# Performance work log

Hardware: AMD Instinct MI355X
Metric: run time of the kernel (lower is better)

The kernel has to match this reference:

```python
import jax, jax.numpy as jnp
import numpy as np

B, C_IN, C_OUT, H, W, K = 8, 32, 32, 96, 96, 5


def setup_inputs() -> dict:
    key = jax.random.key(0)
    k1, k2 = jax.random.split(key)
    f = jax.random.normal(k1, (B, C_IN, H, W), dtype=jnp.float32)
    # xavier_uniform-style init for the structuring element h
    fan_in = C_IN * K * K
    fan_out = C_OUT * K * K
    bound = float(np.sqrt(6.0 / (fan_in + fan_out)))
    h = jax.random.uniform(k2, (C_OUT, C_IN, K, K), dtype=jnp.float32,
                           minval=-bound, maxval=bound)
    return {"f": f, "h": h}


def reference(f, h):
    """Morphological max-plus dilation with 'same' padding.

    out[b,o,y,x] = max_{c,i,j} f[b,c,y+i-p, x+j-p] + h[o,c,i,j]
    """
    b, c, hh, ww = f.shape
    o, _, k, _ = h.shape
    p = k // 2
    neg = -jnp.finfo(f.dtype).max / 2
    fp = jnp.pad(f, ((0, 0), (0, 0), (p, p), (p, p)), constant_values=neg)
    out = jnp.full((b, o, hh, ww), neg, dtype=f.dtype)
    for i in range(k):          # fixed small kernel loop (k*k = 25 taps)
        for j in range(k):
            sl = fp[:, :, i:i + hh, j:j + ww]              # (B, C, H, W)
            w_ij = h[:, :, i, j]                            # (O, C)
            # max-plus over input channels: (B,1,C,H,W) + (O,C,1,1)
            cand = jnp.max(sl[:, None] + w_ij[None, :, :, None, None], axis=2)
            out = jnp.maximum(out, cand)
    return out
```

## Files before the change

kernel.cpp:

```cpp
#include <hip/hip_runtime.h>


#define B_ 8
#define C_ 32
#define O_ 32
#define H_ 96
#define W_ 96
#define K_ 5
#define KK_ (K_ * K_)
#define NCP_ (C_ / 2)

#define TX_ 24
#define RT_ 8
#define CS_ 2
#define TY_ (RT_ * CS_)
#define NT_ (TX_ * TY_)
#define XR_ 4
#define OB_ 4
#define CPG_ (NCP_ / CS_)

#define PH_ 100
#define PW_ 104
#define PLSZ_ (PH_ * PW_)
#define FPAD_BYTES ((size_t)B_ * NCP_ * PLSZ_ * 4)

#define HBLK_ 128
#define HPH_ 24
#define HPACK_DW (8 * NCP_ * HBLK_)

#define NEGF (-30000.0f)

typedef _Float16 h2 __attribute__((ext_vector_type(2)));
typedef int sv8 __attribute__((ext_vector_type(8)));
typedef int sv4 __attribute__((ext_vector_type(4)));
typedef unsigned uv4 __attribute__((ext_vector_type(4)));

static __device__ __forceinline__ h2 h2b(unsigned u) {
    return __builtin_bit_cast(h2, u);
}
static __device__ __forceinline__ unsigned bh2(h2 v) {
    return __builtin_bit_cast(unsigned, v);
}

static __device__ __forceinline__ void pk_addmax_s(h2& acc, h2 fv, int hs) {
    h2 t;
    asm("v_pk_add_f16 %0, %1, %2" : "=v"(t) : "v"(fv), "s"(hs));
    asm("v_pk_max_f16 %0, %1, %2" : "=v"(acc) : "v"(acc), "v"(t));
}

static __device__ __forceinline__ int hget20(sv8 a, sv8 b, sv4 c, int n) {
    if (n < 8)  return a[n];
    if (n < 16) return b[n - 8];
    return c[n - 16];
}

static __device__ __forceinline__ h2 getwin(uv4 a, uv4 b, int d) {
    if (d == 0) return h2b(a[0]);
    if (d == 1) return h2b(a[1]);
    if (d == 2) return h2b(a[2]);
    if (d == 3) return h2b(a[3]);
    if (d == 4) return h2b(b[0]);
    if (d == 5) return h2b(b[1]);
    if (d == 6) return h2b(b[2]);
    return h2b(b[3]);
}

static __device__ __forceinline__ void compute_phase(h2 (&acc)[OB_][XR_],
        uv4 wa, uv4 wb, sv8 c0, sv8 c1, sv4 c2) {
#pragma unroll
    for (int j = 0; j < K_; ++j) {
        const int n = j * 4;
        const int h0 = hget20(c0, c1, c2, n);
        const int h1 = hget20(c0, c1, c2, n + 1);
        const int h2v = hget20(c0, c1, c2, n + 2);
        const int h3 = hget20(c0, c1, c2, n + 3);
#pragma unroll
        for (int xx = 0; xx < XR_; ++xx) {
            h2 fv = getwin(wa, wb, xx + j);
            pk_addmax_s(acc[0][xx], fv, h0);
            pk_addmax_s(acc[1][xx], fv, h1);
            pk_addmax_s(acc[2][xx], fv, h2v);
            pk_addmax_s(acc[3][xx], fv, h3);
        }
    }
}

#define HLOADM(B0, B1, B2, HP, O0S, O1S, O2S)                          \
    asm volatile("s_load_dwordx8 %0, %3, " O0S "\n\t"                  \
                 "s_load_dwordx8 %1, %3, " O1S "\n\t"                  \
                 "s_load_dwordx4 %2, %3, " O2S                         \
                 : "=s"(B0), "=s"(B1), "=s"(B2) : "s"(HP))

#define WLOADM(SA, SB, PTR)                                            \
    asm volatile("global_load_dwordx4 %0, %2, off\n\t"                 \
                 "global_load_dwordx4 %1, %2, off offset:16"           \
                 : "=v"(SA), "=v"(SB) : "v"(PTR))

#define PHASE(CB0, CB1, CB2, NB0, NB1, NB2, NHP, O0S, O1S, O2S, WS, PS, PPTR) \
    do {                                                                      \
        asm volatile("s_waitcnt lgkmcnt(0)"                                   \
                     : "+s"(CB0), "+s"(CB1), "+s"(CB2));                      \
        HLOADM(NB0, NB1, NB2, NHP, O0S, O1S, O2S);                            \
        asm volatile("s_waitcnt vmcnt(6)"                                     \
                     : "+v"(win[WS][0]), "+v"(win[WS][1]));                   \
        WLOADM(win[PS][0], win[PS][1], PPTR);                                 \
        compute_phase(acc, win[WS][0], win[WS][1], CB0, CB1, CB2);            \
    } while (0)

__global__ __launch_bounds__(256)
void prep_kernel(const float* __restrict__ f, const float* __restrict__ h,
                 unsigned* __restrict__ fpad, unsigned* __restrict__ hpack) {
    const int bz = blockIdx.z;
    if (bz < B_) {
        const int idx = blockIdx.x * 256 + threadIdx.x;
        const int cp = blockIdx.y;
        if (idx >= PLSZ_) return;
        const int row = idx / PW_;
        const int col = idx - row * PW_;
        const int y = row - 2;
        const int x = col - 2;
        float v0 = NEGF, v1 = NEGF;
        if ((unsigned)y < H_ && (unsigned)x < W_) {
            v0 = f[((size_t)(bz * C_ + 2 * cp)     * H_ + y) * W_ + x];
            v1 = f[((size_t)(bz * C_ + 2 * cp + 1) * H_ + y) * W_ + x];
        }
        h2 d; d.x = (_Float16)v0; d.y = (_Float16)v1;
        fpad[(size_t)(bz * NCP_ + cp) * PLSZ_ + idx] = bh2(d);
    } else {
        const int t = (blockIdx.y * gridDim.x + blockIdx.x) * 256 + threadIdx.x;
        if (t >= 8 * NCP_ * KK_ * OB_) return;
        const int og = t / (NCP_ * KK_ * OB_);
        int r  = t - og * (NCP_ * KK_ * OB_);
        const int cp = r / (KK_ * OB_);
        r -= cp * (KK_ * OB_);
        const int ij = r / OB_;
        const int o  = r - ij * OB_;
        const int p  = ij / K_;
        const int jj = ij - p * K_;
        float a0 = h[((size_t)(og * OB_ + o) * C_ + 2 * cp)     * KK_ + ij];
        float a1 = h[((size_t)(og * OB_ + o) * C_ + 2 * cp + 1) * KK_ + ij];
        h2 pv; pv.x = (_Float16)a0; pv.y = (_Float16)a1;
        hpack[(size_t)(og * NCP_ + cp) * HBLK_ + p * HPH_ + jj * 4 + o] = bh2(pv);
    }
}

__global__ __launch_bounds__(NT_)
void dilate_main(const unsigned* __restrict__ fpad,
                 const unsigned* __restrict__ hpack,
                 float* __restrict__ out) {
    const int tx  = threadIdx.x;
    const int ty  = threadIdx.y;
    const int ry  = ty & (RT_ - 1);
    const int g   = ty >> 3;
    const int gu  = __builtin_amdgcn_readfirstlane(g);

    const int ytile = blockIdx.x;
    const int og    = blockIdx.y;
    const int b     = blockIdx.z;
    const int y0 = ytile * RT_;
    const int o0 = og * OB_;
    const int x0 = XR_ * tx;
    const int yb = y0 + ry;

    __shared__ unsigned short comb[OB_ * XR_][RT_ * TX_];

    h2 acc[OB_][XR_];
    {
        h2 neg; neg.x = (_Float16)NEGF; neg.y = (_Float16)NEGF;
#pragma unroll
        for (int o = 0; o < OB_; ++o)
#pragma unroll
            for (int xx = 0; xx < XR_; ++xx) acc[o][xx] = neg;
    }

    const int cp0v = g * CPG_;
    const int cp0s = gu * CPG_;
    const unsigned* hpb = hpack + (size_t)(og * NCP_ + cp0s) * HBLK_;
    const unsigned* pvb = fpad + (size_t)(b * NCP_ + cp0v) * PLSZ_ + yb * PW_ + x0;

    sv8 hA0, hA1; sv4 hA2;
    sv8 hB0, hB1; sv4 hB2;
    uv4 win[5][2];

    HLOADM(hA0, hA1, hA2, hpb, "0x0", "0x20", "0x40");
    WLOADM(win[0][0], win[0][1], pvb);
    WLOADM(win[1][0], win[1][1], pvb + PW_);
    WLOADM(win[2][0], win[2][1], pvb + 2 * PW_);
    WLOADM(win[3][0], win[3][1], pvb + 3 * PW_);

#pragma unroll 1
    for (int cpi = 0; cpi < CPG_; cpi += 2) {
        const unsigned* hb0 = hpb + (size_t)cpi * HBLK_;
        const unsigned* hb1 = hb0 + HBLK_;
        const unsigned* hb2 = (cpi + 2 < CPG_) ? hb1 + HBLK_ : hb1;
        const unsigned* pv0 = pvb + (size_t)cpi * PLSZ_;
        const unsigned* pv1 = pv0 + PLSZ_;
        const unsigned* pv2 = (cpi + 2 < CPG_) ? pv1 + PLSZ_ : pv1;

        PHASE(hA0,hA1,hA2, hB0,hB1,hB2, hb0, "0x60","0x80","0xa0",   0, 4, pv0 + 4*PW_);
        PHASE(hB0,hB1,hB2, hA0,hA1,hA2, hb0, "0xc0","0xe0","0x100",  1, 0, pv1);
        PHASE(hA0,hA1,hA2, hB0,hB1,hB2, hb0, "0x120","0x140","0x160",2, 1, pv1 + PW_);
        PHASE(hB0,hB1,hB2, hA0,hA1,hA2, hb0, "0x180","0x1a0","0x1c0",3, 2, pv1 + 2*PW_);
        PHASE(hA0,hA1,hA2, hB0,hB1,hB2, hb1, "0x0","0x20","0x40",    4, 3, pv1 + 3*PW_);
        PHASE(hB0,hB1,hB2, hA0,hA1,hA2, hb1, "0x60","0x80","0xa0",   0, 4, pv1 + 4*PW_);
        PHASE(hA0,hA1,hA2, hB0,hB1,hB2, hb1, "0xc0","0xe0","0x100",  1, 0, pv2);
        PHASE(hB0,hB1,hB2, hA0,hA1,hA2, hb1, "0x120","0x140","0x160",2, 1, pv2 + PW_);
        PHASE(hA0,hA1,hA2, hB0,hB1,hB2, hb1, "0x180","0x1a0","0x1c0",3, 2, pv2 + 2*PW_);
        PHASE(hB0,hB1,hB2, hA0,hA1,hA2, hb2, "0x0","0x20","0x40",    4, 3, pv2 + 3*PW_);
    }

    asm volatile("s_waitcnt vmcnt(0) lgkmcnt(0)"
                 : "+v"(win[0][0]), "+v"(win[0][1]),
                   "+v"(win[1][0]), "+v"(win[1][1]),
                   "+v"(win[2][0]), "+v"(win[2][1]),
                   "+v"(win[3][0]), "+v"(win[3][1]),
                   "+s"(hA0), "+s"(hA1), "+s"(hA2));

    unsigned short red[OB_][XR_];
#pragma unroll
    for (int o = 0; o < OB_; ++o)
#pragma unroll
        for (int xx = 0; xx < XR_; ++xx) {
            _Float16 a = acc[o][xx].x;
            _Float16 b2 = acc[o][xx].y;
            _Float16 m = (a > b2) ? a : b2;
            red[o][xx] = __builtin_bit_cast(unsigned short, m);
        }

    const int t192 = ry * TX_ + tx;
    if (g == 1) {
#pragma unroll
        for (int o = 0; o < OB_; ++o)
#pragma unroll
            for (int xx = 0; xx < XR_; ++xx)
                comb[o * XR_ + xx][t192] = red[o][xx];
    }
    __syncthreads();
    if (g == 0) {
        const int y = yb;
#pragma unroll
        for (int o = 0; o < OB_; ++o) {
            float r[XR_];
#pragma unroll
            for (int xx = 0; xx < XR_; ++xx) {
                _Float16 m  = __builtin_bit_cast(_Float16, red[o][xx]);
                _Float16 v0 = __builtin_bit_cast(_Float16,
                                                 comb[o * XR_ + xx][t192]);
                m = (v0 > m) ? v0 : m;
                r[xx] = (float)m;
            }
            float4 v = make_float4(r[0], r[1], r[2], r[3]);
            *(float4*)&out[(((size_t)b * O_ + (o0 + o)) * H_ + y) * W_ + x0] = v;
        }
    }
}

__global__ __launch_bounds__(256)
void dilate_naive(const float* __restrict__ f, const float* __restrict__ h,
                  float* __restrict__ out) {
    const int idx = blockIdx.x * 256 + threadIdx.x;
    if (idx >= B_ * O_ * H_ * W_) return;
    const int x = idx % W_;
    const int y = (idx / W_) % H_;
    const int o = (idx / (W_ * H_)) % O_;
    const int b = idx / (W_ * H_ * O_);
    float m = -3.0e38f;
    for (int c = 0; c < C_; ++c)
        for (int i = 0; i < K_; ++i)
            for (int j = 0; j < K_; ++j) {
                int yy = y + i - 2, xc = x + j - 2;
                if ((unsigned)yy < H_ && (unsigned)xc < W_) {
                    float v = f[((size_t)(b * C_ + c) * H_ + yy) * W_ + xc] +
                              h[((size_t)o * C_ + c) * KK_ + i * K_ + j];
                    m = fmaxf(m, v);
                }
            }
    out[idx] = m;
}

extern "C" void kernel_launch(void* const* d_in, const int* in_sizes, int n_in,
                              void* d_out, int out_size, void* d_ws, size_t ws_size,
                              hipStream_t stream) {
    const float* f = (const float*)d_in[0];
    const float* h = (const float*)d_in[1];
    float* out = (float*)d_out;

    const size_t need = FPAD_BYTES + (size_t)HPACK_DW * 4;
    if (ws_size >= need) {
        unsigned* fpad  = (unsigned*)d_ws;
        unsigned* hpack = (unsigned*)((char*)d_ws + FPAD_BYTES);
        dim3 pgrid((PLSZ_ + 255) / 256, NCP_, B_ + 1);
        hipLaunchKernelGGL(prep_kernel, pgrid, dim3(256), 0, stream,
                           f, h, fpad, hpack);
        dim3 mgrid(H_ / RT_, O_ / OB_, B_);
        dim3 mblock(TX_, TY_);
        hipLaunchKernelGGL(dilate_main, mgrid, mblock, 0, stream,
                           fpad, hpack, out);
    } else {
        hipLaunchKernelGGL(dilate_naive,
                           dim3((B_ * O_ * H_ * W_ + 255) / 256), dim3(256),
                           0, stream, f, h, out);
    }
}
```

Baseline: 139.5 us.

## Halve output-channel block, shrink window buffering to double-buffer, raise occupancy

Cuts outputs per thread from 4 to 2 channels, doubling the grid along output groups, and replaces the five-deep row-window ring with a two-buffer ping-pong that issues only one row ahead. Loads now use immediate offsets, and the add and max steps are split so adds can be batched. A launch-bounds occupancy hint of 7 is added. The goal is fewer registers and more waves per CU to hide latency, at the cost of loading each input window twice as often across blocks and a shallower prefetch distance.

```diff
diff --git a/kernel.cpp b/kernel.cpp
--- a/kernel.cpp
+++ b/kernel.cpp
@@ -16,7 +16,8 @@
 #define TY_ (RT_ * CS_)
 #define NT_ (TX_ * TY_)
 #define XR_ 4
-#define OB_ 4
+#define OB_ 2
+#define NOG_ (O_ / OB_)
 #define CPG_ (NCP_ / CS_)
 
 #define PH_ 100
@@ -25,14 +26,14 @@
 #define FPAD_BYTES ((size_t)B_ * NCP_ * PLSZ_ * 4)
 
 #define HBLK_ 128
-#define HPH_ 24
-#define HPACK_DW (8 * NCP_ * HBLK_)
+#define HPH_ 16
+#define HPACK_DW (NOG_ * NCP_ * HBLK_)
 
 #define NEGF (-30000.0f)
 
 typedef _Float16 h2 __attribute__((ext_vector_type(2)));
 typedef int sv8 __attribute__((ext_vector_type(8)));
-typedef int sv4 __attribute__((ext_vector_type(4)));
+typedef int sv2 __attribute__((ext_vector_type(2)));
 typedef unsigned uv4 __attribute__((ext_vector_type(4)));
 
 static __device__ __forceinline__ h2 h2b(unsigned u) {
@@ -42,16 +43,18 @@
     return __builtin_bit_cast(unsigned, v);
 }
 
-static __device__ __forceinline__ void pk_addmax_s(h2& acc, h2 fv, int hs) {
+static __device__ __forceinline__ h2 pk_add_s(h2 fv, int hs) {
     h2 t;
     asm("v_pk_add_f16 %0, %1, %2" : "=v"(t) : "v"(fv), "s"(hs));
+    return t;
+}
+static __device__ __forceinline__ void pk_max(h2& acc, h2 t) {
     asm("v_pk_max_f16 %0, %1, %2" : "=v"(acc) : "v"(acc), "v"(t));
 }
 
-static __device__ __forceinline__ int hget20(sv8 a, sv8 b, sv4 c, int n) {
-    if (n < 8)  return a[n];
-    if (n < 16) return b[n - 8];
-    return c[n - 16];
+static __device__ __forceinline__ int hget10(sv8 a, sv2 b, int n) {
+    if (n < 8) return a[n];
+    return b[n - 8];
 }
 
 static __device__ __forceinline__ h2 getwin(uv4 a, uv4 b, int d) {
@@ -66,45 +69,43 @@
 }
 
 static __device__ __forceinline__ void compute_phase(h2 (&acc)[OB_][XR_],
-        uv4 wa, uv4 wb, sv8 c0, sv8 c1, sv4 c2) {
+        uv4 wa, uv4 wb, sv8 c0, sv2 c1) {
 #pragma unroll
     for (int j = 0; j < K_; ++j) {
-        const int n = j * 4;
-        const int h0 = hget20(c0, c1, c2, n);
-        const int h1 = hget20(c0, c1, c2, n + 1);
-        const int h2v = hget20(c0, c1, c2, n + 2);
-        const int h3 = hget20(c0, c1, c2, n + 3);
+        const int h0 = hget10(c0, c1, j * 2);
+        const int h1 = hget10(c0, c1, j * 2 + 1);
+        h2 t[XR_][OB_];
 #pragma unroll
         for (int xx = 0; xx < XR_; ++xx) {
             h2 fv = getwin(wa, wb, xx + j);
-            pk_addmax_s(acc[0][xx], fv, h0);
-            pk_addmax_s(acc[1][xx], fv, h1);
-            pk_addmax_s(acc[2][xx], fv, h2v);
-            pk_addmax_s(acc[3][xx], fv, h3);
-        }
-    }
-}
-
-#define HLOADM(B0, B1, B2, HP, O0S, O1S, O2S)                          \
-    asm volatile("s_load_dwordx8 %0, %3, " O0S "\n\t"                  \
-                 "s_load_dwordx8 %1, %3, " O1S "\n\t"                  \
-                 "s_load_dwordx4 %2, %3, " O2S                         \
-                 : "=s"(B0), "=s"(B1), "=s"(B2) : "s"(HP))
-
-#define WLOADM(SA, SB, PTR)                                            \
-    asm volatile("global_load_dwordx4 %0, %2, off\n\t"                 \
-                 "global_load_dwordx4 %1, %2, off offset:16"           \
+            t[xx][0] = pk_add_s(fv, h0);
+            t[xx][1] = pk_add_s(fv, h1);
+        }
+#pragma unroll
+        for (int xx = 0; xx < XR_; ++xx) {
+            pk_max(acc[0][xx], t[xx][0]);
+            pk_max(acc[1][xx], t[xx][1]);
+        }
+    }
+}
+
+#define HLOADM(B0, B1, HP, O0S, O1S)                                   \
+    asm volatile("s_load_dwordx8 %0, %2, " O0S "\n\t"                  \
+                 "s_load_dwordx2 %1, %2, " O1S                         \
+                 : "=s"(B0), "=s"(B1) : "s"(HP))
+
+#define WLOADM(SA, SB, PTR, O0S, O1S)                                  \
+    asm volatile("global_load_dwordx4 %0, %2, off offset:" O0S "\n\t"  \
+                 "global_load_dwordx4 %1, %2, off offset:" O1S         \
                  : "=v"(SA), "=v"(SB) : "v"(PTR))
 
-#define PHASE(CB0, CB1, CB2, NB0, NB1, NB2, NHP, O0S, O1S, O2S, WS, PS, PPTR) \
-    do {                                                                      \
-        asm volatile("s_waitcnt lgkmcnt(0)"                                   \
-                     : "+s"(CB0), "+s"(CB1), "+s"(CB2));                      \
-        HLOADM(NB0, NB1, NB2, NHP, O0S, O1S, O2S);                            \
-        asm volatile("s_waitcnt vmcnt(6)"                                     \
-                     : "+v"(win[WS][0]), "+v"(win[WS][1]));                   \
-        WLOADM(win[PS][0], win[PS][1], PPTR);                                 \
-        compute_phase(acc, win[WS][0], win[WS][1], CB0, CB1, CB2);            \
+#define PHASE(CH0, CH1, NH0, NH1, NHP, HO0, HO1, CW, NW, NPTR, WO0, WO1) \
+    do {                                                                  \
+        asm volatile("s_waitcnt lgkmcnt(0)" : "+s"(CH0), "+s"(CH1));      \
+        HLOADM(NH0, NH1, NHP, HO0, HO1);                                  \
+        WLOADM(NW[0], NW[1], NPTR, WO0, WO1);                             \
+        asm volatile("s_waitcnt vmcnt(2)" : "+v"(CW[0]), "+v"(CW[1]));    \
+        compute_phase(acc, CW[0], CW[1], CH0, CH1);                       \
     } while (0)
 
 __global__ __launch_bounds__(256)
@@ -128,7 +129,7 @@
         fpad[(size_t)(bz * NCP_ + cp) * PLSZ_ + idx] = bh2(d);
     } else {
         const int t = (blockIdx.y * gridDim.x + blockIdx.x) * 256 + threadIdx.x;
-        if (t >= 8 * NCP_ * KK_ * OB_) return;
+        if (t >= NOG_ * NCP_ * KK_ * OB_) return;
         const int og = t / (NCP_ * KK_ * OB_);
         int r  = t - og * (NCP_ * KK_ * OB_);
         const int cp = r / (KK_ * OB_);
@@ -140,11 +141,11 @@
         float a0 = h[((size_t)(og * OB_ + o) * C_ + 2 * cp)     * KK_ + ij];
         float a1 = h[((size_t)(og * OB_ + o) * C_ + 2 * cp + 1) * KK_ + ij];
         h2 pv; pv.x = (_Float16)a0; pv.y = (_Float16)a1;
-        hpack[(size_t)(og * NCP_ + cp) * HBLK_ + p * HPH_ + jj * 4 + o] = bh2(pv);
-    }
-}
-
-__global__ __launch_bounds__(NT_)
+        hpack[(size_t)(og * NCP_ + cp) * HBLK_ + p * HPH_ + jj * OB_ + o] = bh2(pv);
+    }
+}
+
+__global__ __launch_bounds__(NT_, 7)
 void dilate_main(const unsigned* __restrict__ fpad,
                  const unsigned* __restrict__ hpack,
                  float* __restrict__ out) {
@@ -178,15 +179,12 @@
     const unsigned* hpb = hpack + (size_t)(og * NCP_ + cp0s) * HBLK_;
     const unsigned* pvb = fpad + (size_t)(b * NCP_ + cp0v) * PLSZ_ + yb * PW_ + x0;
 
-    sv8 hA0, hA1; sv4 hA2;
-    sv8 hB0, hB1; sv4 hB2;
-    uv4 win[5][2];
-
-    HLOADM(hA0, hA1, hA2, hpb, "0x0", "0x20", "0x40");
-    WLOADM(win[0][0], win[0][1], pvb);
-    WLOADM(win[1][0], win[1][1], pvb + PW_);
-    WLOADM(win[2][0], win[2][1], pvb + 2 * PW_);
-    WLOADM(win[3][0], win[3][1], pvb + 3 * PW_);
+    sv8 hA0; sv2 hA1;
+    sv8 hB0; sv2 hB1;
+    uv4 winA[2], winB[2];
+
+    HLOADM(hA0, hA1, hpb, "0x0", "0x20");
+    WLOADM(winA[0], winA[1], pvb, "0", "16");
 
 #pragma unroll 1
     for (int cpi = 0; cpi < CPG_; cpi += 2) {
@@ -197,24 +195,20 @@
         const unsigned* pv1 = pv0 + PLSZ_;
         const unsigned* pv2 = (cpi + 2 < CPG_) ? pv1 + PLSZ_ : pv1;
 
-        PHASE(hA0,hA1,hA2, hB0,hB1,hB2, hb0, "0x60","0x80","0xa0",   0, 4, pv0 + 4*PW_);
-        PHASE(hB0,hB1,hB2, hA0,hA1,hA2, hb0, "0xc0","0xe0","0x100",  1, 0, pv1);
-        PHASE(hA0,hA1,hA2, hB0,hB1,hB2, hb0, "0x120","0x140","0x160",2, 1, pv1 + PW_);
-        PHASE(hB0,hB1,hB2, hA0,hA1,hA2, hb0, "0x180","0x1a0","0x1c0",3, 2, pv1 + 2*PW_);
-        PHASE(hA0,hA1,hA2, hB0,hB1,hB2, hb1, "0x0","0x20","0x40",    4, 3, pv1 + 3*PW_);
-        PHASE(hB0,hB1,hB2, hA0,hA1,hA2, hb1, "0x60","0x80","0xa0",   0, 4, pv1 + 4*PW_);
-        PHASE(hA0,hA1,hA2, hB0,hB1,hB2, hb1, "0xc0","0xe0","0x100",  1, 0, pv2);
-        PHASE(hB0,hB1,hB2, hA0,hA1,hA2, hb1, "0x120","0x140","0x160",2, 1, pv2 + PW_);
-        PHASE(hA0,hA1,hA2, hB0,hB1,hB2, hb1, "0x180","0x1a0","0x1c0",3, 2, pv2 + 2*PW_);
-        PHASE(hB0,hB1,hB2, hA0,hA1,hA2, hb2, "0x0","0x20","0x40",    4, 3, pv2 + 3*PW_);
+        PHASE(hA0,hA1, hB0,hB1, hb0, "0x40","0x60",   winA, winB, pv0, "416","432");
+        PHASE(hB0,hB1, hA0,hA1, hb0, "0x80","0xa0",   winB, winA, pv0, "832","848");
+        PHASE(hA0,hA1, hB0,hB1, hb0, "0xc0","0xe0",   winA, winB, pv0, "1248","1264");
+        PHASE(hB0,hB1, hA0,hA1, hb0, "0x100","0x120", winB, winA, pv0, "1664","1680");
+        PHASE(hA0,hA1, hB0,hB1, hb1, "0x0","0x20",    winA, winB, pv1, "0","16");
+        PHASE(hB0,hB1, hA0,hA1, hb1, "0x40","0x60",   winB, winA, pv1, "416","432");
+        PHASE(hA0,hA1, hB0,hB1, hb1, "0x80","0xa0",   winA, winB, pv1, "832","848");
+        PHASE(hB0,hB1, hA0,hA1, hb1, "0xc0","0xe0",   winB, winA, pv1, "1248","1264");
+        PHASE(hA0,hA1, hB0,hB1, hb1, "0x100","0x120", winA, winB, pv1, "1664","1680");
+        PHASE(hB0,hB1, hA0,hA1, hb2, "0x0","0x20",    winB, winA, pv2, "0","16");
     }
 
     asm volatile("s_waitcnt vmcnt(0) lgkmcnt(0)"
-                 : "+v"(win[0][0]), "+v"(win[0][1]),
-                   "+v"(win[1][0]), "+v"(win[1][1]),
-                   "+v"(win[2][0]), "+v"(win[2][1]),
-                   "+v"(win[3][0]), "+v"(win[3][1]),
-                   "+s"(hA0), "+s"(hA1), "+s"(hA2));
+                 : "+v"(winA[0]), "+v"(winA[1]), "+s"(hA0), "+s"(hA1));
 
     unsigned short red[OB_][XR_];
 #pragma unroll
@@ -292,7 +286,7 @@
         dim3 pgrid((PLSZ_ + 255) / 256, NCP_, B_ + 1);
         hipLaunchKernelGGL(prep_kernel, pgrid, dim3(256), 0, stream,
                            f, h, fpad, hpack);
-        dim3 mgrid(H_ / RT_, O_ / OB_, B_);
+        dim3 mgrid(H_ / RT_, NOG_, B_);
         dim3 mblock(TX_, TY_);
         hipLaunchKernelGGL(dilate_main, mgrid, mblock, 0, stream,
                            fpad, hpack, out);
```

Measured after the change: 134.3 us (median of 2 runs). -3.7%, faster.
